# Kernel tuning notes

Measured on AMD Instinct MI355X. Metric: run time of the kernel, lower is better.

## Reference

```python
import jax, jax.numpy as jnp
import numpy as np

N_ATOMS = 100000
N_EDGES = 3200000
N_RBF = 8
HIDDEN = 16
NUM_GRAPHS = 1


def setup_inputs() -> dict:
    key = jax.random.key(0)
    ks = jax.random.split(key, 10)
    positions = jax.random.normal(ks[0], (N_ATOMS, 3), dtype=jnp.float32)
    vectors = jax.random.normal(ks[1], (N_EDGES, 3), dtype=jnp.float32)
    local_or_ghost = jax.random.uniform(ks[2], (N_ATOMS,), dtype=jnp.float32)
    W1 = jax.random.normal(ks[3], (N_RBF, HIDDEN), dtype=jnp.float32) * 0.1
    b1 = jax.random.normal(ks[4], (HIDDEN,), dtype=jnp.float32) * 0.1
    W2 = jax.random.normal(ks[5], (HIDDEN, HIDDEN), dtype=jnp.float32) * 0.1
    w3 = jax.random.normal(ks[6], (HIDDEN,), dtype=jnp.float32) * 0.1
    field = jax.random.normal(ks[7], (3,), dtype=jnp.float32) * 0.01
    alphas = jax.random.uniform(ks[8], (N_RBF,), dtype=jnp.float32, minval=0.1, maxval=1.1)
    edge_index = jax.random.randint(ks[9], (2, N_EDGES), 0, N_ATOMS, dtype=jnp.int64)
    batch = jnp.zeros((N_ATOMS,), dtype=jnp.int64)
    return {"positions": positions, "vectors": vectors, "local_or_ghost": local_or_ghost,
            "W1": W1, "b1": b1, "W2": W2, "w3": w3, "field": field, "alphas": alphas,
            "edge_index": edge_index, "batch": batch}


def _node_energy(positions, vectors, W1, b1, W2, w3, field, alphas, receiver, n_atoms):
    # Surrogate MACE-like energy: radial basis on edge vectors -> edge MLP ->
    # scatter to receiving atom -> node MLP, plus a linear position term.
    r2 = jnp.sum(vectors * vectors, axis=-1)              # (E,)
    phi = jnp.exp(-r2[:, None] * alphas[None, :])         # (E, F)
    msg = jax.nn.silu(phi @ W1 + b1)                      # (E, H)
    h = jax.ops.segment_sum(msg, receiver, num_segments=n_atoms)  # (N, H)
    node_e = jax.nn.silu(h @ W2) @ w3 + positions @ field          # (N,)
    return node_e


def reference(positions, vectors, local_or_ghost, W1, b1, W2, w3, field, alphas, edge_index, batch):
    n_atoms = positions.shape[0]
    sender, receiver = edge_index[0], edge_index[1]

    def total_local(pos, vec):
        ne = _node_energy(pos, vec, W1, b1, W2, w3, field, alphas, receiver, n_atoms)
        return jnp.sum(ne * local_or_ghost), ne

    # forces = -dE/dpositions, edge_forces = -dE/dvectors (vectors as independent leaf)
    (_, node_energy), grads = jax.value_and_grad(total_local, argnums=(0, 1), has_aux=True)(positions, vectors)
    forces = -grads[0]
    edge_forces = -grads[1]

    node_energy_local = node_energy * local_or_ghost
    total_energy_local = jax.ops.segment_sum(node_energy_local, batch, num_segments=NUM_GRAPHS)

    # edge virial: einsum('zi,zj->zij')
    edge_virial = edge_forces[:, :, None] * vectors[:, None, :]   # (E, 3, 3)
    av_send = jax.ops.segment_sum(edge_virial, sender, num_segments=n_atoms)
    av_recv = jax.ops.segment_sum(edge_virial, receiver, num_segments=n_atoms)
    atom_virial = (av_send + av_recv) * 0.5
    atom_virial = (atom_virial + jnp.swapaxes(atom_virial, -1, -2)) * 0.5
    atom_virial = -atom_virial
    virials = jnp.sum(atom_virial, axis=0)                        # (3, 3)

    return total_energy_local, node_energy, forces, virials, atom_virial
```

## Files before the change

### kernel.cpp

```cpp
#include <hip/hip_runtime.h>

#define N_ATOMS 100000
#define N_EDGES 3200000
#define N_RBF 8
#define HIDDEN 16

#define NB 4096
#define TSCALE 64.0f

#define OFF_TE   0
#define OFF_NE   1
#define OFF_F    (1 + N_ATOMS)
#define OFF_VIR  (1 + N_ATOMS + 3*N_ATOMS)
#define OFF_AV   (OFF_VIR + 9)

#define WPAD (N_ATOMS + 4)
#define NBLK16 (N_ATOMS / 16)
#define SCAN_B 1024
#define SCAN_NB ((N_ATOMS + SCAN_B) / SCAN_B)

#define NTAB_S   0
#define NTAB_G   (NB*HIDDEN)
#define NOFF_R   (2*NB*HIDDEN)
#define NOFF_S   (NOFF_R + WPAD)
#define NCNT_R8  (NOFF_S + WPAD)
#define NCNT_S8  (NCNT_R8 + 8*WPAD)
#define NRANK_R  (NCNT_S8 + 8*WPAD)
#define NRANK_S  (NRANK_R + N_EDGES)
#define NDR2     NRANK_R
#define NBSUM    NRANK_R
#define NAV6     NRANK_S
#define NTEP     (NRANK_S + 6*N_ATOMS)
#define NVPART   (NTEP + 8192)
#define NPAY_R   (NRANK_S + N_EDGES)
#define NPAY_S   (NPAY_R + 4*N_EDGES)
#define NEND     (NPAY_S + 4*N_EDGES)

#define WOFF_OFFS_R 0
#define WOFF_OFFS_S WPAD
#define WOFF_RANK_R (2*WPAD)
#define WOFF_RANK_S (WOFF_RANK_R + N_EDGES)
#define WOFF_EID_R  (WOFF_RANK_S + N_EDGES)
#define WOFF_EID_S  (WOFF_EID_R + N_EDGES)
#define WOFF_DR2    (WOFF_EID_S + N_EDGES)
#define WOFF_AV6    (WOFF_DR2 + N_EDGES)
#define WOFF_END    (WOFF_AV6 + 6*N_ATOMS)

typedef float fvec4 __attribute__((ext_vector_type(4)));

__device__ inline void nt_store4(float a, float b, float c, float d, float4* p) {
    fvec4 t;
    t.x = a; t.y = b; t.z = c; t.w = d;
    __builtin_nontemporal_store(t, (fvec4*)p);
}

__global__ void build_tables(const float* __restrict__ W1, const float* __restrict__ b1,
                             const float* __restrict__ alphas,
                             float* __restrict__ s_tab, float* __restrict__ g_tab) {
    int idx = blockIdx.x * blockDim.x + threadIdx.x;
    int b = idx >> 4, j = idx & 15;
    float r2 = (float)b / TSCALE;
    float pre = b1[j], pw = 0.f;
    #pragma unroll
    for (int f = 0; f < N_RBF; ++f) {
        float al = alphas[f];
        float ph = __expf(-r2 * al);
        float w  = W1[f*HIDDEN + j];
        pre += ph * w;
        pw  += al * ph * w;
    }
    float sig = 1.f / (1.f + __expf(-pre));
    s_tab[idx] = pre * sig;
    g_tab[idx] = sig * (1.f + pre * (1.f - sig)) * pw;
}


__global__ void count8_kernel(const int* __restrict__ ei,
                              int* __restrict__ cnt_r8, int* __restrict__ cnt_s8) {
    unsigned int xcd;
    asm volatile("s_getreg_b32 %0, hwreg(HW_REG_XCC_ID)" : "=s"(xcd));
    xcd &= 7;
    int e = blockIdx.x * blockDim.x + threadIdx.x;
    if (e >= N_EDGES) return;
    int send = ei[e], recv = ei[N_EDGES + e];
    __hip_atomic_fetch_add(&cnt_r8[xcd * WPAD + recv], 1,
                           __ATOMIC_RELAXED, __HIP_MEMORY_SCOPE_WORKGROUP);
    __hip_atomic_fetch_add(&cnt_s8[xcd * WPAD + send], 1,
                           __ATOMIC_RELAXED, __HIP_MEMORY_SCOPE_WORKGROUP);
}

__global__ void xcd_prefix_kernel(int* __restrict__ cnt_r8, int* __restrict__ cnt_s8,
                                  int* __restrict__ offs_r, int* __restrict__ offs_s) {
    int a = blockIdx.x * blockDim.x + threadIdx.x;
    if (a >= N_ATOMS) return;
    int t = 0;
    #pragma unroll
    for (int x = 0; x < 8; ++x) {
        int c = cnt_r8[x*WPAD + a];
        cnt_r8[x*WPAD + a] = t;
        t += c;
    }
    offs_r[a] = t;
    t = 0;
    #pragma unroll
    for (int x = 0; x < 8; ++x) {
        int c = cnt_s8[x*WPAD + a];
        cnt_s8[x*WPAD + a] = t;
        t += c;
    }
    offs_s[a] = t;
}


__global__ void scanA(int* __restrict__ offs_r, int* __restrict__ offs_s,
                      int* __restrict__ bsum) {
    int y = blockIdx.y;
    int* a = y ? offs_s : offs_r;
    const int n = N_ATOMS + 1;
    int i = blockIdx.x * SCAN_B + threadIdx.x;
    int v = (i < n) ? a[i] : 0;
    int lane = threadIdx.x & 63, w = threadIdx.x >> 6;
    int s = v;
    #pragma unroll
    for (int o = 1; o < 64; o <<= 1) {
        int t = __shfl_up(s, o);
        if (lane >= o) s += t;
    }
    __shared__ int wsum[16];
    if (lane == 63) wsum[w] = s;
    __syncthreads();
    if (threadIdx.x < 16) {
        int ws = wsum[threadIdx.x];
        int sc = ws;
        #pragma unroll
        for (int o = 1; o < 16; o <<= 1) {
            int t = __shfl_up(sc, o);
            if ((int)threadIdx.x >= o) sc += t;
        }
        wsum[threadIdx.x] = sc;
    }
    __syncthreads();
    int wpre = (w > 0) ? wsum[w-1] : 0;
    int excl = s - v + wpre;
    if (i < n) a[i] = excl;
    if (threadIdx.x == 0) bsum[y * SCAN_NB + blockIdx.x] = wsum[15];
}

__global__ void scanB(int* __restrict__ bsum) {
    __shared__ int lds[SCAN_NB];
    for (int y = 0; y < 2; ++y) {
        if (threadIdx.x < SCAN_NB) lds[threadIdx.x] = bsum[y*SCAN_NB + threadIdx.x];
        __syncthreads();
        if (threadIdx.x == 0) {
            int run = 0;
            for (int i = 0; i < SCAN_NB; ++i) { int t = lds[i]; lds[i] = run; run += t; }
        }
        __syncthreads();
        if (threadIdx.x < SCAN_NB) bsum[y*SCAN_NB + threadIdx.x] = lds[threadIdx.x];
        __syncthreads();
    }
}

__global__ void scanC(int* __restrict__ offs_r, int* __restrict__ offs_s,
                      const int* __restrict__ bsum) {
    int y = blockIdx.y;
    int* a = y ? offs_s : offs_r;
    int i = blockIdx.x * SCAN_B + threadIdx.x;
    if (i < N_ATOMS + 1) a[i] += bsum[y*SCAN_NB + blockIdx.x];
}

__global__ void scatter2(const int* __restrict__ ei,
                         const int* __restrict__ offs_r, const int* __restrict__ offs_s,
                         int* __restrict__ cnt_r8, int* __restrict__ cnt_s8,
                         const float* __restrict__ vectors,
                         float4* __restrict__ pay_r, float4* __restrict__ pay_s) {
    unsigned int xcd;
    asm volatile("s_getreg_b32 %0, hwreg(HW_REG_XCC_ID)" : "=s"(xcd));
    xcd &= 7;
    int e = blockIdx.x * blockDim.x + threadIdx.x;
    if (e >= N_EDGES) return;
    int send = ei[e], recv = ei[N_EDGES + e];
    int br = __hip_atomic_fetch_add(&cnt_r8[xcd*WPAD + recv], 1,
                                    __ATOMIC_RELAXED, __HIP_MEMORY_SCOPE_WORKGROUP);
    int rs = offs_r[recv] + br;
    int bs = __hip_atomic_fetch_add(&cnt_s8[xcd*WPAD + send], 1,
                                    __ATOMIC_RELAXED, __HIP_MEMORY_SCOPE_WORKGROUP);
    int ss = offs_s[send] + bs;
    float vx = vectors[3*e], vy = vectors[3*e+1], vz = vectors[3*e+2];
    float r2 = vx*vx + vy*vy + vz*vz;
    nt_store4(vx, vy, vz, __int_as_float(ss), &pay_r[rs]);
    nt_store4(vx, vy, vz, r2, &pay_s[ss]);
}


__global__ void fused16(const float4* __restrict__ pay_r,
                        const float* __restrict__ positions,
                        const float* __restrict__ lg,
                        const float* __restrict__ W2, const float* __restrict__ w3,
                        const float* __restrict__ field,
                        const int* __restrict__ offs_r,
                        const float* __restrict__ s_tab, const float* __restrict__ g_tab,
                        float* __restrict__ dr2_s, float* __restrict__ av6,
                        float* __restrict__ tepart, float* __restrict__ out) {
    int tid = blockIdx.x * blockDim.x + threadIdx.x;
    int a = tid >> 4;
    int sl = threadIdx.x & 15;
    int lane = threadIdx.x & 63;
    int gb = lane & 48;
    int start = offs_r[a], end = offs_r[a + 1];
    int k0 = start + sl;

    float m[HIDDEN];
    #pragma unroll
    for (int j = 0; j < HIDDEN; ++j) m[j] = 0.f;

    for (int k = k0; k < end; k += 16) {
        float4 p = pay_r[k];
        float r2 = p.x*p.x + p.y*p.y + p.z*p.z;
        float x = fminf(r2 * TSCALE, (float)(NB - 2) + 0.999f);
        int i = (int)x;
        float f = x - (float)i;
        const float4* r0 = (const float4*)(s_tab + i * HIDDEN);
        const float4* r1 = (const float4*)(s_tab + (i + 1) * HIDDEN);
        #pragma unroll
        for (int q = 0; q < 4; ++q) {
            float4 A = r0[q], B = r1[q];
            m[4*q+0] += A.x + f * (B.x - A.x);
            m[4*q+1] += A.y + f * (B.y - A.y);
            m[4*q+2] += A.z + f * (B.z - A.z);
            m[4*q+3] += A.w + f * (B.w - A.w);
        }
    }

    #pragma unroll
    for (int o = 1; o < 16; o <<= 1) {
        #pragma unroll
        for (int j = 0; j < HIDDEN; ++j) m[j] += __shfl_xor(m[j], o);
    }

    float aj = 0.f;
    #pragma unroll
    for (int i = 0; i < HIDDEN; ++i) aj += m[i] * W2[i*HIDDEN + sl];
    float sigj = 1.f / (1.f + __expf(-aj));
    float l = lg[a];
    float w3j = w3[sl];
    float sd = aj * sigj * w3j;
    #pragma unroll
    for (int o = 1; o < 16; o <<= 1) sd += __shfl_xor(sd, o);
    float dAj = l * w3j * sigj * (1.f + aj * (1.f - sigj));
    float gown = 0.f;
    #pragma unroll
    for (int q = 0; q < HIDDEN; ++q) {
        float dq = __shfl(dAj, gb | q);
        gown += dq * W2[sl*HIDDEN + q];
    }
    float g[HIDDEN];
    #pragma unroll
    for (int q = 0; q < HIDDEN; ++q) g[q] = __shfl(gown, gb | q);

    float contrib = 0.f;
    if (sl == 0) {
        float ne = sd + positions[3*a]*field[0] + positions[3*a+1]*field[1]
                      + positions[3*a+2]*field[2];
        out[OFF_NE + a] = ne;
        out[OFF_F + 3*a + 0] = -l * field[0];
        out[OFF_F + 3*a + 1] = -l * field[1];
        out[OFF_F + 3*a + 2] = -l * field[2];
        contrib = ne * l;
    }

    float axx=0.f, axy=0.f, axz=0.f, ayy=0.f, ayz=0.f, azz=0.f;
    for (int k = k0; k < end; k += 16) {
        float4 p = pay_r[k];
        float r2 = p.x*p.x + p.y*p.y + p.z*p.z;
        float x = fminf(r2 * TSCALE, (float)(NB - 2) + 0.999f);
        int i = (int)x;
        float f = x - (float)i;
        const float4* r0 = (const float4*)(g_tab + i * HIDDEN);
        const float4* r1 = (const float4*)(g_tab + (i + 1) * HIDDEN);
        float dr2 = 0.f;
        #pragma unroll
        for (int q = 0; q < 4; ++q) {
            float4 A = r0[q], B = r1[q];
            dr2 -= g[4*q+0] * (A.x + f * (B.x - A.x));
            dr2 -= g[4*q+1] * (A.y + f * (B.y - A.y));
            dr2 -= g[4*q+2] * (A.z + f * (B.z - A.z));
            dr2 -= g[4*q+3] * (A.w + f * (B.w - A.w));
        }
        int ss = __float_as_int(p.w);
        __builtin_nontemporal_store(dr2, &dr2_s[ss]);
        axx += dr2*p.x*p.x; axy += dr2*p.x*p.y; axz += dr2*p.x*p.z;
        ayy += dr2*p.y*p.y; ayz += dr2*p.y*p.z; azz += dr2*p.z*p.z;
    }
    #pragma unroll
    for (int o = 1; o < 16; o <<= 1) {
        axx += __shfl_xor(axx, o); axy += __shfl_xor(axy, o); axz += __shfl_xor(axz, o);
        ayy += __shfl_xor(ayy, o); ayz += __shfl_xor(ayz, o); azz += __shfl_xor(azz, o);
    }
    if (sl == 0) {
        float2* p = (float2*)(av6 + (size_t)a * 6);
        p[0] = make_float2(axx, axy);
        p[1] = make_float2(axz, ayy);
        p[2] = make_float2(ayz, azz);
    }

    __shared__ float red[4];
    if (sl != 0) contrib = 0.f;
    contrib += __shfl_xor(contrib, 16);
    contrib += __shfl_xor(contrib, 32);
    int w = threadIdx.x >> 6;
    if (lane == 0) red[w] = contrib;
    __syncthreads();
    if (threadIdx.x == 0) tepart[blockIdx.x] = red[0]+red[1]+red[2]+red[3];
}


__global__ void bwd_send16(const float4* __restrict__ pay_s,
                           const int* __restrict__ offs_s,
                           const float* __restrict__ dr2_s, const float* __restrict__ av6,
                           float* __restrict__ vpart, float* __restrict__ out) {
    int tid = blockIdx.x * blockDim.x + threadIdx.x;
    int a = tid >> 4;
    int sl = threadIdx.x & 15;
    int start = offs_s[a], end = offs_s[a + 1];
    float axx=0.f, axy=0.f, axz=0.f, ayy=0.f, ayz=0.f, azz=0.f;
    for (int k = start + sl; k < end; k += 16) {
        float4 p = pay_s[k];
        float dr2 = dr2_s[k];
        axx += dr2*p.x*p.x; axy += dr2*p.x*p.y; axz += dr2*p.x*p.z;
        ayy += dr2*p.y*p.y; ayz += dr2*p.y*p.z; azz += dr2*p.z*p.z;
    }
    #pragma unroll
    for (int o = 1; o < 16; o <<= 1) {
        axx += __shfl_xor(axx, o); axy += __shfl_xor(axy, o); axz += __shfl_xor(axz, o);
        ayy += __shfl_xor(ayy, o); ayz += __shfl_xor(ayz, o); azz += __shfl_xor(azz, o);
    }
    __shared__ float sh6[16][6];
    int grp = threadIdx.x >> 4;
    if (sl == 0) {
        const float2* p = (const float2*)(av6 + (size_t)a * 6);
        float2 p0 = p[0], p1 = p[1], p2 = p[2];
        axx += p0.x; axy += p0.y; axz += p1.x;
        ayy += p1.y; ayz += p2.x; azz += p2.y;
        float* o9 = out + OFF_AV + (size_t)a * 9;
        o9[0] = axx; o9[1] = axy; o9[2] = axz;
        o9[3] = axy; o9[4] = ayy; o9[5] = ayz;
        o9[6] = axz; o9[7] = ayz; o9[8] = azz;
        sh6[grp][0] = axx; sh6[grp][1] = axy; sh6[grp][2] = axz;
        sh6[grp][3] = ayy; sh6[grp][4] = ayz; sh6[grp][5] = azz;
    }
    __syncthreads();
    if (threadIdx.x < 6) {
        float s = 0.f;
        #pragma unroll
        for (int q = 0; q < 16; ++q) s += sh6[q][threadIdx.x];
        vpart[blockIdx.x * 6 + threadIdx.x] = s;
    }
}


__global__ void finalize_kernel(const float* __restrict__ tepart,
                                const float* __restrict__ vpart,
                                float* __restrict__ out) {
    int t = threadIdx.x;
    float acc[7];
    #pragma unroll
    for (int c = 0; c < 7; ++c) acc[c] = 0.f;
    for (int i = t; i < NBLK16; i += 1024) {
        acc[0] += tepart[i];
        const float* p = vpart + (size_t)i * 6;
        acc[1] += p[0]; acc[2] += p[1]; acc[3] += p[2];
        acc[4] += p[3]; acc[5] += p[4]; acc[6] += p[5];
    }
    #pragma unroll
    for (int c = 0; c < 7; ++c) {
        #pragma unroll
        for (int o = 1; o < 64; o <<= 1) acc[c] += __shfl_xor(acc[c], o);
    }
    __shared__ float sh[16][8];
    int lane = t & 63, w = t >> 6;
    if (lane == 0) {
        #pragma unroll
        for (int c = 0; c < 7; ++c) sh[w][c] = acc[c];
    }
    __syncthreads();
    if (t == 0) {
        float s[7];
        #pragma unroll
        for (int c = 0; c < 7; ++c) {
            float v = 0.f;
            #pragma unroll
            for (int q = 0; q < 16; ++q) v += sh[q][c];
            s[c] = v;
        }
        out[OFF_TE] = s[0];
        out[OFF_VIR + 0] = s[1]; out[OFF_VIR + 1] = s[2]; out[OFF_VIR + 2] = s[3];
        out[OFF_VIR + 3] = s[2]; out[OFF_VIR + 4] = s[4]; out[OFF_VIR + 5] = s[5];
        out[OFF_VIR + 6] = s[3]; out[OFF_VIR + 7] = s[5]; out[OFF_VIR + 8] = s[6];
    }
}


__global__ void count_kernel(const int* __restrict__ ei,
                             int* __restrict__ cnt_r, int* __restrict__ cnt_s,
                             int* __restrict__ rank_r, int* __restrict__ rank_s) {
    int e = blockIdx.x * blockDim.x + threadIdx.x;
    if (e >= N_EDGES) return;
    int send = ei[e], recv = ei[N_EDGES + e];
    rank_r[e] = atomicAdd(&cnt_r[recv], 1);
    rank_s[e] = atomicAdd(&cnt_s[send], 1);
}

__global__ void scan_kernel(int* __restrict__ offs_r, int* __restrict__ offs_s) {
    int* a = (blockIdx.x == 0) ? offs_r : offs_s;
    const int n = N_ATOMS + 1;
    __shared__ int wsum[4];
    __shared__ int carry_s;
    if (threadIdx.x == 0) carry_s = 0;
    __syncthreads();
    int lane = threadIdx.x & 63, w = threadIdx.x >> 6;
    for (int base = 0; base < n; base += 256) {
        int i = base + threadIdx.x;
        int v = (i < n) ? a[i] : 0;
        int s = v;
        #pragma unroll
        for (int o = 1; o < 64; o <<= 1) {
            int t = __shfl_up(s, o);
            if (lane >= o) s += t;
        }
        if (lane == 63) wsum[w] = s;
        __syncthreads();
        int wpre = 0;
        for (int k = 0; k < w; ++k) wpre += wsum[k];
        int incl = s + wpre;
        int total = wsum[0] + wsum[1] + wsum[2] + wsum[3];
        int excl = incl - v + carry_s;
        if (i < n) a[i] = excl;
        __syncthreads();
        if (threadIdx.x == 0) carry_s += total;
        __syncthreads();
    }
}

__global__ void scatter_kernel(const int* __restrict__ ei,
                               const int* __restrict__ offs_r, const int* __restrict__ offs_s,
                               const int* __restrict__ rank_r, const int* __restrict__ rank_s,
                               int* __restrict__ eid_r, int* __restrict__ eid_s) {
    int e = blockIdx.x * blockDim.x + threadIdx.x;
    if (e >= N_EDGES) return;
    int send = ei[e], recv = ei[N_EDGES + e];
    eid_r[offs_r[recv] + rank_r[e]] = e;
    eid_s[offs_s[send] + rank_s[e]] = e;
}

__global__ void fused_kernel(const float* __restrict__ vectors,
                             const float* __restrict__ positions,
                             const float* __restrict__ lg,
                             const float* __restrict__ W1, const float* __restrict__ b1,
                             const float* __restrict__ W2, const float* __restrict__ w3,
                             const float* __restrict__ field, const float* __restrict__ alphas,
                             const int* __restrict__ offs_r, const int* __restrict__ eid_r,
                             float* __restrict__ dr2buf, float* __restrict__ av6,
                             float* __restrict__ out) {
    int a = (blockIdx.x * blockDim.x + threadIdx.x) >> 6;
    int lane = threadIdx.x & 63;
    int start = offs_r[a], end = offs_r[a + 1];
    float al[N_RBF];
    #pragma unroll
    for (int f = 0; f < N_RBF; ++f) al[f] = alphas[f];
    float m[HIDDEN];
    #pragma unroll
    for (int j = 0; j < HIDDEN; ++j) m[j] = 0.f;
    float t[HIDDEN], paw[HIDDEN];
    float vx0 = 0.f, vy0 = 0.f, vz0 = 0.f;
    int e0 = -1;
    int k0 = start + lane;
    for (int k = k0; k < end; k += 64) {
        int e = eid_r[k];
        float vx = vectors[3*e], vy = vectors[3*e+1], vz = vectors[3*e+2];
        float r2 = vx*vx + vy*vy + vz*vz;
        float phi[N_RBF], apf[N_RBF];
        #pragma unroll
        for (int f = 0; f < N_RBF; ++f) { phi[f] = __expf(-r2 * al[f]); apf[f] = al[f] * phi[f]; }
        bool first = (k == k0);
        if (first) { e0 = e; vx0 = vx; vy0 = vy; vz0 = vz; }
        #pragma unroll
        for (int j = 0; j < HIDDEN; ++j) {
            float pre = b1[j];
            float pw = 0.f;
            #pragma unroll
            for (int f = 0; f < N_RBF; ++f) {
                float w = W1[f*HIDDEN + j];
                pre += phi[f] * w;
                pw  += apf[f] * w;
            }
            float sig = 1.f / (1.f + __expf(-pre));
            m[j] += pre * sig;
            if (first) { t[j] = sig * (1.f + pre * (1.f - sig)); paw[j] = pw; }
        }
    }
    #pragma unroll
    for (int o = 1; o < 64; o <<= 1) {
        #pragma unroll
        for (int j = 0; j < HIDDEN; ++j) m[j] += __shfl_xor(m[j], o);
    }
    int jj = lane & 15;
    int gbase = lane & 48;
    float aj = 0.f;
    #pragma unroll
    for (int i = 0; i < HIDDEN; ++i) aj += m[i] * W2[i*HIDDEN + jj];
    float sigj = 1.f / (1.f + __expf(-aj));
    float l = lg[a];
    float sd = aj * sigj * w3[jj];
    #pragma unroll
    for (int o = 1; o < 16; o <<= 1) sd += __shfl_xor(sd, o);
    float dAj = l * w3[jj] * sigj * (1.f + aj * (1.f - sigj));
    float dAv[HIDDEN];
    #pragma unroll
    for (int q = 0; q < HIDDEN; ++q) dAv[q] = __shfl(dAj, gbase | q);
    float gown = 0.f;
    #pragma unroll
    for (int j2 = 0; j2 < HIDDEN; ++j2) gown += dAv[j2] * W2[jj*HIDDEN + j2];
    float g[HIDDEN];
    #pragma unroll
    for (int q = 0; q < HIDDEN; ++q) g[q] = __shfl(gown, gbase | q);
    float contrib = 0.f;
    if (lane == 0) {
        float ne = sd + positions[3*a]*field[0] + positions[3*a+1]*field[1]
                      + positions[3*a+2]*field[2];
        out[OFF_NE + a] = ne;
        out[OFF_F + 3*a + 0] = -l * field[0];
        out[OFF_F + 3*a + 1] = -l * field[1];
        out[OFF_F + 3*a + 2] = -l * field[2];
        contrib = ne * l;
    }
    float axx=0.f, axy=0.f, axz=0.f, ayy=0.f, ayz=0.f, azz=0.f;
    if (k0 < end) {
        float dr2 = 0.f;
        #pragma unroll
        for (int j = 0; j < HIDDEN; ++j) dr2 -= (g[j] * t[j]) * paw[j];
        dr2buf[e0] = dr2;
        axx = dr2*vx0*vx0; axy = dr2*vx0*vy0; axz = dr2*vx0*vz0;
        ayy = dr2*vy0*vy0; ayz = dr2*vy0*vz0; azz = dr2*vz0*vz0;
    }
    for (int k = k0 + 64; k < end; k += 64) {
        int e = eid_r[k];
        float vx = vectors[3*e], vy = vectors[3*e+1], vz = vectors[3*e+2];
        float r2 = vx*vx + vy*vy + vz*vz;
        float phi[N_RBF], apf[N_RBF];
        #pragma unroll
        for (int f = 0; f < N_RBF; ++f) { phi[f] = __expf(-r2 * al[f]); apf[f] = al[f] * phi[f]; }
        float dr2 = 0.f;
        #pragma unroll
        for (int j = 0; j < HIDDEN; ++j) {
            float pre = b1[j];
            float pw = 0.f;
            #pragma unroll
            for (int f = 0; f < N_RBF; ++f) {
                float w = W1[f*HIDDEN + j];
                pre += phi[f] * w;
                pw  += apf[f] * w;
            }
            float sig = 1.f / (1.f + __expf(-pre));
            float tt = sig * (1.f + pre * (1.f - sig));
            dr2 -= (g[j] * tt) * pw;
        }
        dr2buf[e] = dr2;
        axx += dr2*vx*vx; axy += dr2*vx*vy; axz += dr2*vx*vz;
        ayy += dr2*vy*vy; ayz += dr2*vy*vz; azz += dr2*vz*vz;
    }
    #pragma unroll
    for (int o = 1; o < 64; o <<= 1) {
        axx += __shfl_xor(axx, o); axy += __shfl_xor(axy, o); axz += __shfl_xor(axz, o);
        ayy += __shfl_xor(ayy, o); ayz += __shfl_xor(ayz, o); azz += __shfl_xor(azz, o);
    }
    if (lane == 0) {
        float2* p = (float2*)(av6 + (size_t)a * 6);
        p[0] = make_float2(axx, axy);
        p[1] = make_float2(axz, ayy);
        p[2] = make_float2(ayz, azz);
    }
    __shared__ float red[4];
    int w = threadIdx.x >> 6;
    if (lane == 0) red[w] = contrib;
    __syncthreads();
    if (threadIdx.x == 0) atomicAdd(&out[OFF_TE], red[0]+red[1]+red[2]+red[3]);
}

__global__ void bwd_send_kernel(const float* __restrict__ vectors,
                                const int* __restrict__ offs_s, const int* __restrict__ eid_s,
                                const float* __restrict__ dr2buf, const float* __restrict__ av6,
                                float* __restrict__ out) {
    int a = (blockIdx.x * blockDim.x + threadIdx.x) >> 6;
    int lane = threadIdx.x & 63;
    int start = offs_s[a], end = offs_s[a + 1];
    float axx=0.f, axy=0.f, axz=0.f, ayy=0.f, ayz=0.f, azz=0.f;
    for (int k = start + lane; k < end; k += 64) {
        int e = eid_s[k];
        float dr2 = dr2buf[e];
        float vx = vectors[3*e], vy = vectors[3*e+1], vz = vectors[3*e+2];
        axx += dr2*vx*vx; axy += dr2*vx*vy; axz += dr2*vx*vz;
        ayy += dr2*vy*vy; ayz += dr2*vy*vz; azz += dr2*vz*vz;
    }
    #pragma unroll
    for (int o = 1; o < 64; o <<= 1) {
        axx += __shfl_xor(axx, o); axy += __shfl_xor(axy, o); axz += __shfl_xor(axz, o);
        ayy += __shfl_xor(ayy, o); ayz += __shfl_xor(ayz, o); azz += __shfl_xor(azz, o);
    }
    if (lane == 0) {
        const float2* p = (const float2*)(av6 + (size_t)a * 6);
        float2 p0 = p[0], p1 = p[1], p2 = p[2];
        axx += p0.x; axy += p0.y; axz += p1.x;
        ayy += p1.y; ayz += p2.x; azz += p2.y;
        float* o9 = out + OFF_AV + (size_t)a * 9;
        o9[0] = axx; o9[1] = axy; o9[2] = axz;
        o9[3] = axy; o9[4] = ayy; o9[5] = ayz;
        o9[6] = axz; o9[7] = ayz; o9[8] = azz;
    }
}

__global__ void virial_reduce(float* __restrict__ out) {
    const float* av = out + OFF_AV;
    float acc[9];
    #pragma unroll
    for (int c = 0; c < 9; ++c) acc[c] = 0.0f;
    for (int n = blockIdx.x * blockDim.x + threadIdx.x; n < N_ATOMS;
         n += gridDim.x * blockDim.x) {
        #pragma unroll
        for (int c = 0; c < 9; ++c) acc[c] += av[n*9 + c];
    }
    __shared__ float red[4];
    int lane = threadIdx.x & 63, wid = threadIdx.x >> 6;
    #pragma unroll
    for (int c = 0; c < 9; ++c) {
        float v = acc[c];
        #pragma unroll
        for (int o = 32; o > 0; o >>= 1) v += __shfl_down(v, o);
        if (lane == 0) red[wid] = v;
        __syncthreads();
        if (threadIdx.x == 0) atomicAdd(&out[OFF_VIR + c], red[0]+red[1]+red[2]+red[3]);
        __syncthreads();
    }
}


extern "C" void kernel_launch(void* const* d_in, const int* in_sizes, int n_in,
                              void* d_out, int out_size, void* d_ws, size_t ws_size,
                              hipStream_t stream) {
    const float* positions = (const float*)d_in[0];
    const float* vectors   = (const float*)d_in[1];
    const float* lg        = (const float*)d_in[2];
    const float* W1        = (const float*)d_in[3];
    const float* b1        = (const float*)d_in[4];
    const float* W2        = (const float*)d_in[5];
    const float* w3        = (const float*)d_in[6];
    const float* field     = (const float*)d_in[7];
    const float* alphas    = (const float*)d_in[8];
    const int*   edge_index= (const int*)  d_in[9];
    float* out = (float*)d_out;
    int*   wsi = (int*)d_ws;
    float* wsf = (float*)d_ws;

    dim3 blk(256);
    dim3 egrid((N_EDGES + 255) / 256);
    dim3 g16(NBLK16);

    if (ws_size >= (size_t)NEND * 4) {
        float*  s_tab  = wsf + NTAB_S;
        float*  g_tab  = wsf + NTAB_G;
        int*    offs_r = wsi + NOFF_R;
        int*    offs_s = wsi + NOFF_S;
        int*    cnt_r8 = wsi + NCNT_R8;
        int*    cnt_s8 = wsi + NCNT_S8;
        int*    bsum   = wsi + NBSUM;
        float*  dr2_s  = wsf + NDR2;
        float*  av6    = wsf + NAV6;
        float*  tepart = wsf + NTEP;
        float*  vpart  = wsf + NVPART;
        float4* pay_r  = (float4*)(wsf + NPAY_R);
        float4* pay_s  = (float4*)(wsf + NPAY_S);

        hipMemsetAsync(offs_r, 0, (size_t)18 * WPAD * sizeof(int), stream);

        build_tables<<<dim3(NB*HIDDEN/256), blk, 0, stream>>>(W1, b1, alphas, s_tab, g_tab);
        count8_kernel<<<egrid, blk, 0, stream>>>(edge_index, cnt_r8, cnt_s8);
        xcd_prefix_kernel<<<dim3((N_ATOMS+255)/256), blk, 0, stream>>>(cnt_r8, cnt_s8,
                                                                       offs_r, offs_s);
        scanA<<<dim3(SCAN_NB, 2), dim3(SCAN_B), 0, stream>>>(offs_r, offs_s, bsum);
        scanB<<<dim3(1), dim3(256), 0, stream>>>(bsum);
        scanC<<<dim3(SCAN_NB, 2), dim3(SCAN_B), 0, stream>>>(offs_r, offs_s, bsum);
        scatter2<<<egrid, blk, 0, stream>>>(edge_index, offs_r, offs_s,
                                            cnt_r8, cnt_s8, vectors, pay_r, pay_s);
        fused16<<<g16, blk, 0, stream>>>(pay_r, positions, lg, W2, w3, field,
                                         offs_r, s_tab, g_tab, dr2_s, av6, tepart, out);
        bwd_send16<<<g16, blk, 0, stream>>>(pay_s, offs_s, dr2_s, av6, vpart, out);
        finalize_kernel<<<dim3(1), dim3(1024), 0, stream>>>(tepart, vpart, out);
    } else {
        int*   offs_r = wsi + WOFF_OFFS_R;
        int*   offs_s = wsi + WOFF_OFFS_S;
        int*   rank_r = wsi + WOFF_RANK_R;
        int*   rank_s = wsi + WOFF_RANK_S;
        int*   eid_r  = wsi + WOFF_EID_R;
        int*   eid_s  = wsi + WOFF_EID_S;
        float* dr2buf = wsf + WOFF_DR2;
        float* av6    = wsf + WOFF_AV6;
        dim3 agrid(N_ATOMS / 4);

        hipMemsetAsync(offs_r, 0, (size_t)2 * WPAD * sizeof(int), stream);
        hipMemsetAsync(out + OFF_TE, 0, sizeof(float), stream);
        hipMemsetAsync(out + OFF_VIR, 0, 9 * sizeof(float), stream);

        count_kernel<<<egrid, blk, 0, stream>>>(edge_index, offs_r, offs_s, rank_r, rank_s);
        scan_kernel<<<dim3(2), blk, 0, stream>>>(offs_r, offs_s);
        scatter_kernel<<<egrid, blk, 0, stream>>>(edge_index, offs_r, offs_s,
                                                  rank_r, rank_s, eid_r, eid_s);
        fused_kernel<<<agrid, blk, 0, stream>>>(vectors, positions, lg, W1, b1, W2, w3,
                                                field, alphas, offs_r, eid_r, dr2buf, av6, out);
        bwd_send_kernel<<<agrid, blk, 0, stream>>>(vectors, offs_s, eid_s, dr2buf, av6, out);
        virial_reduce<<<dim3(256), blk, 0, stream>>>(out);
    }
}
```

Baseline: 830.9 us.

## Replace sender-side CSR with per-XCD float atomics for sender virial

Drops the sender-sorted CSR build (count, prefix, scan, scatter to pay_s) and the separate sender-side backward kernel. The receiver-grouped kernel now atomically adds each edge's virial contribution into per-XCD sender accumulators and also adds its own receiver sum there. A small finalize kernel then reduces the 8 XCD copies. This removes a second sort pass and payload traffic, but adds six scattered float atomics per edge, a 48*N_ATOMS memset, and a floating-point summation order that is no longer deterministic.

```diff
diff --git a/kernel.cpp b/kernel.cpp
--- a/kernel.cpp
+++ b/kernel.cpp
@@ -16,25 +16,20 @@
 
 #define WPAD (N_ATOMS + 4)
 #define NBLK16 (N_ATOMS / 16)
+#define AVBLK ((N_ATOMS + 255) / 256)
 #define SCAN_B 1024
 #define SCAN_NB ((N_ATOMS + SCAN_B) / SCAN_B)
 
 #define NTAB_S   0
 #define NTAB_G   (NB*HIDDEN)
 #define NOFF_R   (2*NB*HIDDEN)
-#define NOFF_S   (NOFF_R + WPAD)
-#define NCNT_R8  (NOFF_S + WPAD)
-#define NCNT_S8  (NCNT_R8 + 8*WPAD)
-#define NRANK_R  (NCNT_S8 + 8*WPAD)
-#define NRANK_S  (NRANK_R + N_EDGES)
-#define NDR2     NRANK_R
-#define NBSUM    NRANK_R
-#define NAV6     NRANK_S
-#define NTEP     (NRANK_S + 6*N_ATOMS)
+#define NCNT_R8  (NOFF_R + WPAD)
+#define NTEP     (NCNT_R8 + 8*WPAD)
 #define NVPART   (NTEP + 8192)
-#define NPAY_R   (NRANK_S + N_EDGES)
-#define NPAY_S   (NPAY_R + 4*N_EDGES)
-#define NEND     (NPAY_S + 4*N_EDGES)
+#define NAV6S    (NVPART + 4096)
+#define NPAY_R   (NAV6S + 48*N_ATOMS)
+#define NBSUM    NPAY_R
+#define NEND     (NPAY_R + 4*N_EDGES)
 
 #define WOFF_OFFS_R 0
 #define WOFF_OFFS_S WPAD
@@ -46,12 +41,14 @@
 #define WOFF_AV6    (WOFF_DR2 + N_EDGES)
 #define WOFF_END    (WOFF_AV6 + 6*N_ATOMS)
 
-typedef float fvec4 __attribute__((ext_vector_type(4)));
-
-__device__ inline void nt_store4(float a, float b, float c, float d, float4* p) {
-    fvec4 t;
-    t.x = a; t.y = b; t.z = c; t.w = d;
-    __builtin_nontemporal_store(t, (fvec4*)p);
+__device__ inline unsigned int get_xcd() {
+    unsigned int xcd;
+    asm volatile("s_getreg_b32 %0, hwreg(HW_REG_XCC_ID)" : "=s"(xcd));
+    return xcd & 7;
+}
+
+__device__ inline void l2_atomic_addf(float* p, float v) {
+    __hip_atomic_fetch_add(p, v, __ATOMIC_RELAXED, __HIP_MEMORY_SCOPE_WORKGROUP);
 }
 
 __global__ void build_tables(const float* __restrict__ W1, const float* __restrict__ b1,
@@ -75,22 +72,16 @@
 }
 
 
-__global__ void count8_kernel(const int* __restrict__ ei,
-                              int* __restrict__ cnt_r8, int* __restrict__ cnt_s8) {
-    unsigned int xcd;
-    asm volatile("s_getreg_b32 %0, hwreg(HW_REG_XCC_ID)" : "=s"(xcd));
-    xcd &= 7;
+__global__ void count8_r(const int* __restrict__ ei, int* __restrict__ cnt_r8) {
+    unsigned int xcd = get_xcd();
     int e = blockIdx.x * blockDim.x + threadIdx.x;
     if (e >= N_EDGES) return;
-    int send = ei[e], recv = ei[N_EDGES + e];
+    int recv = ei[N_EDGES + e];
     __hip_atomic_fetch_add(&cnt_r8[xcd * WPAD + recv], 1,
                            __ATOMIC_RELAXED, __HIP_MEMORY_SCOPE_WORKGROUP);
-    __hip_atomic_fetch_add(&cnt_s8[xcd * WPAD + send], 1,
-                           __ATOMIC_RELAXED, __HIP_MEMORY_SCOPE_WORKGROUP);
-}
-
-__global__ void xcd_prefix_kernel(int* __restrict__ cnt_r8, int* __restrict__ cnt_s8,
-                                  int* __restrict__ offs_r, int* __restrict__ offs_s) {
+}
+
+__global__ void xcd_prefix_r(int* __restrict__ cnt_r8, int* __restrict__ offs_r) {
     int a = blockIdx.x * blockDim.x + threadIdx.x;
     if (a >= N_ATOMS) return;
     int t = 0;
@@ -101,21 +92,10 @@
         t += c;
     }
     offs_r[a] = t;
-    t = 0;
-    #pragma unroll
-    for (int x = 0; x < 8; ++x) {
-        int c = cnt_s8[x*WPAD + a];
-        cnt_s8[x*WPAD + a] = t;
-        t += c;
-    }
-    offs_s[a] = t;
-}
-
-
-__global__ void scanA(int* __restrict__ offs_r, int* __restrict__ offs_s,
-                      int* __restrict__ bsum) {
-    int y = blockIdx.y;
-    int* a = y ? offs_s : offs_r;
+}
+
+
+__global__ void scanA(int* __restrict__ a, int* __restrict__ bsum) {
     const int n = N_ATOMS + 1;
     int i = blockIdx.x * SCAN_B + threadIdx.x;
     int v = (i < n) ? a[i] : 0;
@@ -130,8 +110,7 @@
     if (lane == 63) wsum[w] = s;
     __syncthreads();
     if (threadIdx.x < 16) {
-        int ws = wsum[threadIdx.x];
-        int sc = ws;
+        int sc = wsum[threadIdx.x];
         #pragma unroll
         for (int o = 1; o < 16; o <<= 1) {
             int t = __shfl_up(sc, o);
@@ -141,55 +120,40 @@
     }
     __syncthreads();
     int wpre = (w > 0) ? wsum[w-1] : 0;
-    int excl = s - v + wpre;
-    if (i < n) a[i] = excl;
-    if (threadIdx.x == 0) bsum[y * SCAN_NB + blockIdx.x] = wsum[15];
+    if (i < n) a[i] = s - v + wpre;
+    if (threadIdx.x == 0) bsum[blockIdx.x] = wsum[15];
 }
 
 __global__ void scanB(int* __restrict__ bsum) {
     __shared__ int lds[SCAN_NB];
-    for (int y = 0; y < 2; ++y) {
-        if (threadIdx.x < SCAN_NB) lds[threadIdx.x] = bsum[y*SCAN_NB + threadIdx.x];
-        __syncthreads();
-        if (threadIdx.x == 0) {
-            int run = 0;
-            for (int i = 0; i < SCAN_NB; ++i) { int t = lds[i]; lds[i] = run; run += t; }
-        }
-        __syncthreads();
-        if (threadIdx.x < SCAN_NB) bsum[y*SCAN_NB + threadIdx.x] = lds[threadIdx.x];
-        __syncthreads();
-    }
-}
-
-__global__ void scanC(int* __restrict__ offs_r, int* __restrict__ offs_s,
-                      const int* __restrict__ bsum) {
-    int y = blockIdx.y;
-    int* a = y ? offs_s : offs_r;
+    if (threadIdx.x < SCAN_NB) lds[threadIdx.x] = bsum[threadIdx.x];
+    __syncthreads();
+    if (threadIdx.x == 0) {
+        int run = 0;
+        for (int i = 0; i < SCAN_NB; ++i) { int t = lds[i]; lds[i] = run; run += t; }
+    }
+    __syncthreads();
+    if (threadIdx.x < SCAN_NB) bsum[threadIdx.x] = lds[threadIdx.x];
+}
+
+__global__ void scanC(int* __restrict__ a, const int* __restrict__ bsum) {
     int i = blockIdx.x * SCAN_B + threadIdx.x;
-    if (i < N_ATOMS + 1) a[i] += bsum[y*SCAN_NB + blockIdx.x];
-}
-
-__global__ void scatter2(const int* __restrict__ ei,
-                         const int* __restrict__ offs_r, const int* __restrict__ offs_s,
-                         int* __restrict__ cnt_r8, int* __restrict__ cnt_s8,
-                         const float* __restrict__ vectors,
-                         float4* __restrict__ pay_r, float4* __restrict__ pay_s) {
-    unsigned int xcd;
-    asm volatile("s_getreg_b32 %0, hwreg(HW_REG_XCC_ID)" : "=s"(xcd));
-    xcd &= 7;
+    if (i < N_ATOMS + 1) a[i] += bsum[blockIdx.x];
+}
+
+__global__ void scatter_r(const int* __restrict__ ei,
+                          const int* __restrict__ offs_r, int* __restrict__ cnt_r8,
+                          const float* __restrict__ vectors,
+                          float4* __restrict__ pay_r) {
+    unsigned int xcd = get_xcd();
     int e = blockIdx.x * blockDim.x + threadIdx.x;
     if (e >= N_EDGES) return;
     int send = ei[e], recv = ei[N_EDGES + e];
     int br = __hip_atomic_fetch_add(&cnt_r8[xcd*WPAD + recv], 1,
                                     __ATOMIC_RELAXED, __HIP_MEMORY_SCOPE_WORKGROUP);
     int rs = offs_r[recv] + br;
-    int bs = __hip_atomic_fetch_add(&cnt_s8[xcd*WPAD + send], 1,
-                                    __ATOMIC_RELAXED, __HIP_MEMORY_SCOPE_WORKGROUP);
-    int ss = offs_s[send] + bs;
     float vx = vectors[3*e], vy = vectors[3*e+1], vz = vectors[3*e+2];
-    float r2 = vx*vx + vy*vy + vz*vz;
-    nt_store4(vx, vy, vz, __int_as_float(ss), &pay_r[rs]);
-    nt_store4(vx, vy, vz, r2, &pay_s[ss]);
+    pay_r[rs] = make_float4(vx, vy, vz, __int_as_float(send));
 }
 
 
@@ -200,8 +164,10 @@
                         const float* __restrict__ field,
                         const int* __restrict__ offs_r,
                         const float* __restrict__ s_tab, const float* __restrict__ g_tab,
-                        float* __restrict__ dr2_s, float* __restrict__ av6,
+                        float* __restrict__ av6s,
                         float* __restrict__ tepart, float* __restrict__ out) {
+    unsigned int xcd = get_xcd();
+    float* avx = av6s + (size_t)xcd * 6 * N_ATOMS;
     int tid = blockIdx.x * blockDim.x + threadIdx.x;
     int a = tid >> 4;
     int sl = threadIdx.x & 15;
@@ -287,10 +253,14 @@
             dr2 -= g[4*q+2] * (A.z + f * (B.z - A.z));
             dr2 -= g[4*q+3] * (A.w + f * (B.w - A.w));
         }
-        int ss = __float_as_int(p.w);
-        __builtin_nontemporal_store(dr2, &dr2_s[ss]);
-        axx += dr2*p.x*p.x; axy += dr2*p.x*p.y; axz += dr2*p.x*p.z;
-        ayy += dr2*p.y*p.y; ayz += dr2*p.y*p.z; azz += dr2*p.z*p.z;
+        float txx = dr2*p.x*p.x, txy = dr2*p.x*p.y, txz = dr2*p.x*p.z;
+        float tyy = dr2*p.y*p.y, tyz = dr2*p.y*p.z, tzz = dr2*p.z*p.z;
+        int sa = __float_as_int(p.w);
+        float* b = avx + (size_t)sa * 6;
+        l2_atomic_addf(b+0, txx); l2_atomic_addf(b+1, txy); l2_atomic_addf(b+2, txz);
+        l2_atomic_addf(b+3, tyy); l2_atomic_addf(b+4, tyz); l2_atomic_addf(b+5, tzz);
+        axx += txx; axy += txy; axz += txz;
+        ayy += tyy; ayz += tyz; azz += tzz;
     }
     #pragma unroll
     for (int o = 1; o < 16; o <<= 1) {
@@ -298,10 +268,9 @@
         ayy += __shfl_xor(ayy, o); ayz += __shfl_xor(ayz, o); azz += __shfl_xor(azz, o);
     }
     if (sl == 0) {
-        float2* p = (float2*)(av6 + (size_t)a * 6);
-        p[0] = make_float2(axx, axy);
-        p[1] = make_float2(axz, ayy);
-        p[2] = make_float2(ayz, azz);
+        float* b = avx + (size_t)a * 6;
+        l2_atomic_addf(b+0, axx); l2_atomic_addf(b+1, axy); l2_atomic_addf(b+2, axz);
+        l2_atomic_addf(b+3, ayy); l2_atomic_addf(b+4, ayz); l2_atomic_addf(b+5, azz);
     }
 
     __shared__ float red[4];
@@ -315,46 +284,39 @@
 }
 
 
-__global__ void bwd_send16(const float4* __restrict__ pay_s,
-                           const int* __restrict__ offs_s,
-                           const float* __restrict__ dr2_s, const float* __restrict__ av6,
-                           float* __restrict__ vpart, float* __restrict__ out) {
-    int tid = blockIdx.x * blockDim.x + threadIdx.x;
-    int a = tid >> 4;
-    int sl = threadIdx.x & 15;
-    int start = offs_s[a], end = offs_s[a + 1];
-    float axx=0.f, axy=0.f, axz=0.f, ayy=0.f, ayz=0.f, azz=0.f;
-    for (int k = start + sl; k < end; k += 16) {
-        float4 p = pay_s[k];
-        float dr2 = dr2_s[k];
-        axx += dr2*p.x*p.x; axy += dr2*p.x*p.y; axz += dr2*p.x*p.z;
-        ayy += dr2*p.y*p.y; ayz += dr2*p.y*p.z; azz += dr2*p.z*p.z;
-    }
-    #pragma unroll
-    for (int o = 1; o < 16; o <<= 1) {
-        axx += __shfl_xor(axx, o); axy += __shfl_xor(axy, o); axz += __shfl_xor(axz, o);
-        ayy += __shfl_xor(ayy, o); ayz += __shfl_xor(ayz, o); azz += __shfl_xor(azz, o);
-    }
-    __shared__ float sh6[16][6];
-    int grp = threadIdx.x >> 4;
-    if (sl == 0) {
-        const float2* p = (const float2*)(av6 + (size_t)a * 6);
-        float2 p0 = p[0], p1 = p[1], p2 = p[2];
-        axx += p0.x; axy += p0.y; axz += p1.x;
-        ayy += p1.y; ayz += p2.x; azz += p2.y;
+__global__ void av_finalize(const float* __restrict__ av6s,
+                            float* __restrict__ vpart, float* __restrict__ out) {
+    int a = blockIdx.x * blockDim.x + threadIdx.x;
+    float s0=0.f,s1=0.f,s2=0.f,s3=0.f,s4=0.f,s5=0.f;
+    if (a < N_ATOMS) {
+        #pragma unroll
+        for (int x = 0; x < 8; ++x) {
+            const float2* p = (const float2*)(av6s + (size_t)x*6*N_ATOMS + (size_t)a*6);
+            float2 p0 = p[0], p1 = p[1], p2 = p[2];
+            s0 += p0.x; s1 += p0.y; s2 += p1.x;
+            s3 += p1.y; s4 += p2.x; s5 += p2.y;
+        }
         float* o9 = out + OFF_AV + (size_t)a * 9;
-        o9[0] = axx; o9[1] = axy; o9[2] = axz;
-        o9[3] = axy; o9[4] = ayy; o9[5] = ayz;
-        o9[6] = axz; o9[7] = ayz; o9[8] = azz;
-        sh6[grp][0] = axx; sh6[grp][1] = axy; sh6[grp][2] = axz;
-        sh6[grp][3] = ayy; sh6[grp][4] = ayz; sh6[grp][5] = azz;
+        o9[0] = s0; o9[1] = s1; o9[2] = s2;
+        o9[3] = s1; o9[4] = s3; o9[5] = s4;
+        o9[6] = s2; o9[7] = s4; o9[8] = s5;
+    }
+    float acc[6] = {s0,s1,s2,s3,s4,s5};
+    int lane = threadIdx.x & 63, w = threadIdx.x >> 6;
+    #pragma unroll
+    for (int c = 0; c < 6; ++c) {
+        #pragma unroll
+        for (int o = 1; o < 64; o <<= 1) acc[c] += __shfl_xor(acc[c], o);
+    }
+    __shared__ float sh[4][6];
+    if (lane == 0) {
+        #pragma unroll
+        for (int c = 0; c < 6; ++c) sh[w][c] = acc[c];
     }
     __syncthreads();
     if (threadIdx.x < 6) {
-        float s = 0.f;
-        #pragma unroll
-        for (int q = 0; q < 16; ++q) s += sh6[q][threadIdx.x];
-        vpart[blockIdx.x * 6 + threadIdx.x] = s;
+        vpart[blockIdx.x * 6 + threadIdx.x] =
+            sh[0][threadIdx.x] + sh[1][threadIdx.x] + sh[2][threadIdx.x] + sh[3][threadIdx.x];
     }
 }
 
@@ -366,8 +328,8 @@
     float acc[7];
     #pragma unroll
     for (int c = 0; c < 7; ++c) acc[c] = 0.f;
-    for (int i = t; i < NBLK16; i += 1024) {
-        acc[0] += tepart[i];
+    for (int i = t; i < NBLK16; i += 1024) acc[0] += tepart[i];
+    for (int i = t; i < AVBLK; i += 1024) {
         const float* p = vpart + (size_t)i * 6;
         acc[1] += p[0]; acc[2] += p[1]; acc[3] += p[2];
         acc[4] += p[3]; acc[5] += p[4]; acc[6] += p[5];
@@ -669,31 +631,26 @@
         float*  s_tab  = wsf + NTAB_S;
         float*  g_tab  = wsf + NTAB_G;
         int*    offs_r = wsi + NOFF_R;
-        int*    offs_s = wsi + NOFF_S;
         int*    cnt_r8 = wsi + NCNT_R8;
-        int*    cnt_s8 = wsi + NCNT_S8;
-        int*    bsum   = wsi + NBSUM;
-        float*  dr2_s  = wsf + NDR2;
-        float*  av6    = wsf + NAV6;
         float*  tepart = wsf + NTEP;
         float*  vpart  = wsf + NVPART;
+        float*  av6s   = wsf + NAV6S;
         float4* pay_r  = (float4*)(wsf + NPAY_R);
-        float4* pay_s  = (float4*)(wsf + NPAY_S);
-
-        hipMemsetAsync(offs_r, 0, (size_t)18 * WPAD * sizeof(int), stream);
+        int*    bsum   = wsi + NBSUM;
+
+        hipMemsetAsync(offs_r, 0, (size_t)9 * WPAD * sizeof(int), stream);
+        hipMemsetAsync(av6s, 0, (size_t)48 * N_ATOMS * sizeof(float), stream);
 
         build_tables<<<dim3(NB*HIDDEN/256), blk, 0, stream>>>(W1, b1, alphas, s_tab, g_tab);
-        count8_kernel<<<egrid, blk, 0, stream>>>(edge_index, cnt_r8, cnt_s8);
-        xcd_prefix_kernel<<<dim3((N_ATOMS+255)/256), blk, 0, stream>>>(cnt_r8, cnt_s8,
-                                                                       offs_r, offs_s);
-        scanA<<<dim3(SCAN_NB, 2), dim3(SCAN_B), 0, stream>>>(offs_r, offs_s, bsum);
-        scanB<<<dim3(1), dim3(256), 0, stream>>>(bsum);
-        scanC<<<dim3(SCAN_NB, 2), dim3(SCAN_B), 0, stream>>>(offs_r, offs_s, bsum);
-        scatter2<<<egrid, blk, 0, stream>>>(edge_index, offs_r, offs_s,
-                                            cnt_r8, cnt_s8, vectors, pay_r, pay_s);
+        count8_r<<<egrid, blk, 0, stream>>>(edge_index, cnt_r8);
+        xcd_prefix_r<<<dim3((N_ATOMS+255)/256), blk, 0, stream>>>(cnt_r8, offs_r);
+        scanA<<<dim3(SCAN_NB), dim3(SCAN_B), 0, stream>>>(offs_r, bsum);
+        scanB<<<dim3(1), dim3(128), 0, stream>>>(bsum);
+        scanC<<<dim3(SCAN_NB), dim3(SCAN_B), 0, stream>>>(offs_r, bsum);
+        scatter_r<<<egrid, blk, 0, stream>>>(edge_index, offs_r, cnt_r8, vectors, pay_r);
         fused16<<<g16, blk, 0, stream>>>(pay_r, positions, lg, W2, w3, field,
-                                         offs_r, s_tab, g_tab, dr2_s, av6, tepart, out);
-        bwd_send16<<<g16, blk, 0, stream>>>(pay_s, offs_s, dr2_s, av6, vpart, out);
+                                         offs_r, s_tab, g_tab, av6s, tepart, out);
+        av_finalize<<<dim3(AVBLK), blk, 0, stream>>>(av6s, vpart, out);
         finalize_kernel<<<dim3(1), dim3(1024), 0, stream>>>(tepart, vpart, out);
     } else {
         int*   offs_r = wsi + WOFF_OFFS_R;
```

After: 1.322 ms. 1.59x slower.
